# Optimization experiments

Measured on AMD Instinct MI355X. Metric: run time of the kernel, lower is better.

The kernel has to match this reference:

```python
import jax, jax.numpy as jnp
import numpy as np

N_NODES = 50000
N_EDGES = 800000
IN_CH = 128
OUT_CH = 64
HID_CH = 2 * OUT_CH  # 128


def gcn_conv(x, edge_index, W, b, n_nodes):
    """PyG GCNConv: linear -> add self-loops -> sym-normalized scatter-add -> bias."""
    h = x @ W  # [N, out]
    loop = jnp.arange(n_nodes)
    row = jnp.concatenate([edge_index[0], loop])  # source nodes
    col = jnp.concatenate([edge_index[1], loop])  # target nodes
    deg = jax.ops.segment_sum(jnp.ones_like(col, dtype=h.dtype), col, num_segments=n_nodes)
    dinv = jnp.where(deg > 0, jax.lax.rsqrt(jnp.maximum(deg, 1.0)), 0.0)
    norm = dinv[row] * dinv[col]  # [E+N]
    msg = h[row] * norm[:, None]  # gather + scale, [E+N, out]
    out = jax.ops.segment_sum(msg, col, num_segments=n_nodes)  # scatter-add
    return out + b


def setup_inputs() -> dict:
    key = jax.random.key(0)
    ks = jax.random.split(key, 9)
    x = jax.random.normal(ks[0], (N_NODES, IN_CH), dtype=jnp.float32)
    edge_index = jax.random.randint(ks[1], (2, N_EDGES), 0, N_NODES, dtype=jnp.int64)
    s_in = 1.0 / np.sqrt(IN_CH)
    s_hid = 1.0 / np.sqrt(HID_CH)
    W1 = jax.random.normal(ks[2], (IN_CH, HID_CH), dtype=jnp.float32) * s_in
    b1 = jnp.zeros((HID_CH,), dtype=jnp.float32)
    W2 = jax.random.normal(ks[3], (HID_CH, OUT_CH), dtype=jnp.float32) * s_hid
    b2 = jnp.zeros((OUT_CH,), dtype=jnp.float32)
    W3 = jax.random.normal(ks[4], (HID_CH, OUT_CH), dtype=jnp.float32) * s_hid
    b3 = jnp.zeros((OUT_CH,), dtype=jnp.float32)
    return {"x": x, "edge_index": edge_index, "W1": W1, "b1": b1,
            "W2": W2, "b2": b2, "W3": W3, "b3": b3}


def reference(x, edge_index, W1, b1, W2, b2, W3, b3):
    act = jax.nn.relu
    hidden = act(gcn_conv(x, edge_index, W1, b1, N_NODES))
    x1 = act(gcn_conv(hidden, edge_index, W2, b2, N_NODES))
    x2 = act(gcn_conv(hidden, edge_index, W3, b3, N_NODES))
    return (x1, x2)
```

## Files before the change

### kernel.cpp

```cpp
#include <hip/hip_runtime.h>

#define N_NODES 50000
#define N_EDGES 800000
#define CH 128
#define WT_PAD 136
#define DUMMY N_NODES
#define SLOT_LOG 6
#define AGG_HALF_BLKS 1563

typedef __attribute__((ext_vector_type(8))) short short8;
typedef __attribute__((ext_vector_type(4))) float floatx4;

__device__ __forceinline__ short f2bf(float f) {
    union { float f; unsigned u; } v; v.f = f;
    unsigned r = v.u + 0x7fff + ((v.u >> 16) & 1);
    return (short)(r >> 16);
}
__device__ __forceinline__ float bflo(unsigned u) {
    union { unsigned u; float f; } v; v.u = u << 16; return v.f;
}
__device__ __forceinline__ float bfhi(unsigned u) {
    union { unsigned u; float f; } v; v.u = u & 0xffff0000u; return v.f;
}


__global__ __launch_bounds__(256) void prep_kernel(const float* __restrict__ W1,
                                                   const float* __restrict__ W2,
                                                   const float* __restrict__ W3,
                                                   const float* __restrict__ b2,
                                                   const float* __restrict__ b3,
                                                   unsigned short* __restrict__ Wt1,
                                                   unsigned short* __restrict__ Wt23,
                                                   float* __restrict__ b23,
                                                   int* __restrict__ counts,
                                                   float* __restrict__ dinv,
                                                   unsigned int* __restrict__ gdummy) {
    int i = blockIdx.x * blockDim.x + threadIdx.x;
    if (i < 128 * 128) {
        int n = i >> 7, k = i & 127;
        Wt1[i] = (unsigned short)f2bf(W1[k * 128 + n]);
        float w = (n < 64) ? W2[k * 64 + n] : W3[k * 64 + (n - 64)];
        Wt23[i] = (unsigned short)f2bf(w);
    } else if (i < 128 * 128 + 128) {
        int k2 = i - 128 * 128;
        b23[k2] = (k2 < 64) ? b2[k2] : b3[k2 - 64];
    } else if (i < 128 * 128 + 192) {
        gdummy[i - (128 * 128 + 128)] = 0;
    }
    for (int j = i; j < N_NODES; j += 66 * 256) {
        counts[j] = 0;
        dinv[j] = 1.0f;
    }
}


__global__ void rank_kernel(const int* __restrict__ ei, int* __restrict__ counts,
                            unsigned* __restrict__ rankdst) {
    int e = blockIdx.x * blockDim.x + threadIdx.x;
    if (e < N_EDGES) {
        int dst = ei[N_EDGES + e];
        int r = atomicAdd(&counts[dst], 1);
        rankdst[e] = ((unsigned)r << 16) | (unsigned)dst;
    }
}

__global__ void scatter_plain(const int* __restrict__ ei, const int* __restrict__ counts,
                              const unsigned* __restrict__ rankdst,
                              unsigned short* __restrict__ sorted_src,
                              float* __restrict__ dinv) {
    int e = blockIdx.x * blockDim.x + threadIdx.x;
    if (e < N_EDGES) {
        int src = ei[e];
        unsigned p = rankdst[e];
        int dst = (int)(p & 0xffffu);
        int r = (int)(p >> 16);
        int deg = counts[dst];
        int base = dst << SLOT_LOG;
        if (r < 64) sorted_src[base + r] = (unsigned short)src;
        if (r == 0) dinv[dst] = rsqrtf((float)(deg + 1));
        if (r == deg - 1) {
            int pc = (deg + 3) & ~3;
            if (pc > 64) pc = 64;
            for (int q = deg; q < pc; ++q) sorted_src[base + q] = (unsigned short)DUMMY;
        }
    }
}


template <bool A_BF16>
__global__ __launch_bounds__(256) void gemm_mfma(const void* __restrict__ Ain,
                                                 const unsigned short* __restrict__ Wt,
                                                 const float* __restrict__ dinv,
                                                 unsigned short* __restrict__ g) {
    __shared__ unsigned short lds[128 * WT_PAD];
    int tid = threadIdx.x;
    int wave = tid >> 6, lane = tid & 63;
    int quad = lane >> 4, ln = lane & 15;

    {
        int r = tid >> 1, h = tid & 1;
        const int4* src = (const int4*)(Wt + r * 128 + h * 64);
#pragma unroll
        for (int i = 0; i < 8; ++i)
            *(int4*)&lds[r * WT_PAD + h * 64 + i * 8] = src[i];
    }

    int row_base = blockIdx.x * 64 + wave * 16;
    int arow = row_base + ln;
    bool ok = arow < N_NODES;
    short8 afrag[4];
    if (A_BF16) {
        const unsigned short* A = (const unsigned short*)Ain;
#pragma unroll
        for (int kk = 0; kk < 4; ++kk) {
            short8 v = {};
            if (ok) v = *(const short8*)(A + arow * 128 + kk * 32 + quad * 8);
            afrag[kk] = v;
        }
    } else {
        const float* A = (const float*)Ain;
#pragma unroll
        for (int kk = 0; kk < 4; ++kk) {
            short8 v = {};
            if (ok) {
                const float* p = A + arow * 128 + kk * 32 + quad * 8;
#pragma unroll
                for (int j = 0; j < 8; ++j) v[j] = f2bf(p[j]);
            }
            afrag[kk] = v;
        }
    }
    __syncthreads();

    floatx4 acc[8] = {};
#pragma unroll
    for (int n0 = 0; n0 < 8; ++n0) {
#pragma unroll
        for (int kk = 0; kk < 4; ++kk) {
            short8 b = *(const short8*)&lds[(n0 * 16 + ln) * WT_PAD + kk * 32 + quad * 8];
            acc[n0] = __builtin_amdgcn_mfma_f32_16x16x32_bf16(afrag[kk], b, acc[n0], 0, 0, 0);
        }
    }

    __syncthreads();
    unsigned short* st = &lds[wave * 16 * WT_PAD];
    float dv[4];
#pragma unroll
    for (int r = 0; r < 4; ++r) {
        int node = row_base + quad * 4 + r;
        dv[r] = (node < N_NODES) ? dinv[node] : 0.f;
    }
#pragma unroll
    for (int n0 = 0; n0 < 8; ++n0)
#pragma unroll
        for (int r = 0; r < 4; ++r)
            st[(quad * 4 + r) * WT_PAD + n0 * 16 + ln] =
                (unsigned short)f2bf(acc[n0][r] * dv[r]);
    __syncthreads();

#pragma unroll
    for (int i = 0; i < 4; ++i) {
        int row = i * 4 + quad;
        int node = row_base + row;
        short8 v = *(const short8*)&st[row * WT_PAD + ln * 8];
        if (node < N_NODES) *(short8*)(g + node * 128 + ln * 8) = v;
    }
}


template <int MODE>
__global__ __launch_bounds__(256) void aggregate_bf16(const unsigned short* __restrict__ g,
                                                      const float* __restrict__ dinv,
                                                      const int* __restrict__ degs,
                                                      const unsigned short* __restrict__ srcs,
                                                      const float* __restrict__ bias,
                                                      void* __restrict__ outp) {
    int h = 0, nb = blockIdx.x;
    if (nb >= AGG_HALF_BLKS) { h = 1; nb -= AGG_HALF_BLKS; }
    int n = nb * 32 + (threadIdx.x >> 3);
    if (n >= N_NODES) return;
    int c4 = threadIdx.x & 7;
    int hoff = h * 8;
    const uint4* grow = (const uint4*)g;
    uint4 u = grow[n * 16 + hoff + c4];
    float a0 = bflo(u.x), a1 = bfhi(u.x), a2 = bflo(u.y), a3 = bfhi(u.y);
    float a4 = bflo(u.z), a5 = bfhi(u.z), a6 = bflo(u.w), a7 = bfhi(u.w);
    float c0 = 0.f, c1 = 0.f, c2 = 0.f, c3 = 0.f, c5 = 0.f, c6 = 0.f, c7 = 0.f, c8 = 0.f;
    int beg = n << SLOT_LOG;
    int pend = beg + ((degs[n] + 3) & ~3);
    int e = beg;
    for (; e + 8 <= pend; e += 8) {
        ushort4 sa = *(const ushort4*)&srcs[e];
        ushort4 sb = *(const ushort4*)&srcs[e + 4];
        uint4 v0 = grow[sa.x * 16 + hoff + c4];
        uint4 v1 = grow[sa.y * 16 + hoff + c4];
        uint4 v2 = grow[sa.z * 16 + hoff + c4];
        uint4 v3 = grow[sa.w * 16 + hoff + c4];
        uint4 v4 = grow[sb.x * 16 + hoff + c4];
        uint4 v5 = grow[sb.y * 16 + hoff + c4];
        uint4 v6 = grow[sb.z * 16 + hoff + c4];
        uint4 v7 = grow[sb.w * 16 + hoff + c4];
        a0 += bflo(v0.x); a1 += bfhi(v0.x); a2 += bflo(v0.y); a3 += bfhi(v0.y);
        a4 += bflo(v0.z); a5 += bfhi(v0.z); a6 += bflo(v0.w); a7 += bfhi(v0.w);
        c0 += bflo(v1.x); c1 += bfhi(v1.x); c2 += bflo(v1.y); c3 += bfhi(v1.y);
        c5 += bflo(v1.z); c6 += bfhi(v1.z); c7 += bflo(v1.w); c8 += bfhi(v1.w);
        a0 += bflo(v2.x); a1 += bfhi(v2.x); a2 += bflo(v2.y); a3 += bfhi(v2.y);
        a4 += bflo(v2.z); a5 += bfhi(v2.z); a6 += bflo(v2.w); a7 += bfhi(v2.w);
        c0 += bflo(v3.x); c1 += bfhi(v3.x); c2 += bflo(v3.y); c3 += bfhi(v3.y);
        c5 += bflo(v3.z); c6 += bfhi(v3.z); c7 += bflo(v3.w); c8 += bfhi(v3.w);
        a0 += bflo(v4.x); a1 += bfhi(v4.x); a2 += bflo(v4.y); a3 += bfhi(v4.y);
        a4 += bflo(v4.z); a5 += bfhi(v4.z); a6 += bflo(v4.w); a7 += bfhi(v4.w);
        c0 += bflo(v5.x); c1 += bfhi(v5.x); c2 += bflo(v5.y); c3 += bfhi(v5.y);
        c5 += bflo(v5.z); c6 += bfhi(v5.z); c7 += bflo(v5.w); c8 += bfhi(v5.w);
        a0 += bflo(v6.x); a1 += bfhi(v6.x); a2 += bflo(v6.y); a3 += bfhi(v6.y);
        a4 += bflo(v6.z); a5 += bfhi(v6.z); a6 += bflo(v6.w); a7 += bfhi(v6.w);
        c0 += bflo(v7.x); c1 += bfhi(v7.x); c2 += bflo(v7.y); c3 += bfhi(v7.y);
        c5 += bflo(v7.z); c6 += bfhi(v7.z); c7 += bflo(v7.w); c8 += bfhi(v7.w);
    }
    if (e < pend) {
        ushort4 sa = *(const ushort4*)&srcs[e];
        uint4 v0 = grow[sa.x * 16 + hoff + c4];
        uint4 v1 = grow[sa.y * 16 + hoff + c4];
        uint4 v2 = grow[sa.z * 16 + hoff + c4];
        uint4 v3 = grow[sa.w * 16 + hoff + c4];
        a0 += bflo(v0.x); a1 += bfhi(v0.x); a2 += bflo(v0.y); a3 += bfhi(v0.y);
        a4 += bflo(v0.z); a5 += bfhi(v0.z); a6 += bflo(v0.w); a7 += bfhi(v0.w);
        c0 += bflo(v1.x); c1 += bfhi(v1.x); c2 += bflo(v1.y); c3 += bfhi(v1.y);
        c5 += bflo(v1.z); c6 += bfhi(v1.z); c7 += bflo(v1.w); c8 += bfhi(v1.w);
        a0 += bflo(v2.x); a1 += bfhi(v2.x); a2 += bflo(v2.y); a3 += bfhi(v2.y);
        a4 += bflo(v2.z); a5 += bfhi(v2.z); a6 += bflo(v2.w); a7 += bfhi(v2.w);
        c0 += bflo(v3.x); c1 += bfhi(v3.x); c2 += bflo(v3.y); c3 += bfhi(v3.y);
        c5 += bflo(v3.z); c6 += bfhi(v3.z); c7 += bflo(v3.w); c8 += bfhi(v3.w);
    }
    a0 += c0; a1 += c1; a2 += c2; a3 += c3; a4 += c5; a5 += c6; a6 += c7; a7 += c8;
    float d = dinv[n];
    float4 bv0 = ((const float4*)bias)[h * 16 + c4 * 2];
    float4 bv1 = ((const float4*)bias)[h * 16 + c4 * 2 + 1];
    float o0 = fmaxf(d * a0 + bv0.x, 0.f);
    float o1 = fmaxf(d * a1 + bv0.y, 0.f);
    float o2 = fmaxf(d * a2 + bv0.z, 0.f);
    float o3 = fmaxf(d * a3 + bv0.w, 0.f);
    float o4 = fmaxf(d * a4 + bv1.x, 0.f);
    float o5 = fmaxf(d * a5 + bv1.y, 0.f);
    float o6 = fmaxf(d * a6 + bv1.z, 0.f);
    float o7 = fmaxf(d * a7 + bv1.w, 0.f);
    if (MODE == 0) {
        uint4 w;
        w.x = ((unsigned)(unsigned short)f2bf(o0)) | (((unsigned)(unsigned short)f2bf(o1)) << 16);
        w.y = ((unsigned)(unsigned short)f2bf(o2)) | (((unsigned)(unsigned short)f2bf(o3)) << 16);
        w.z = ((unsigned)(unsigned short)f2bf(o4)) | (((unsigned)(unsigned short)f2bf(o5)) << 16);
        w.w = ((unsigned)(unsigned short)f2bf(o6)) | (((unsigned)(unsigned short)f2bf(o7)) << 16);
        ((uint4*)outp)[n * 16 + hoff + c4] = w;
    } else {
        float* out = (float*)outp + (size_t)h * N_NODES * 64;
        ((float4*)out)[n * 16 + c4 * 2] = make_float4(o0, o1, o2, o3);
        ((float4*)out)[n * 16 + c4 * 2 + 1] = make_float4(o4, o5, o6, o7);
    }
}


extern "C" void kernel_launch(void* const* d_in, const int* in_sizes, int n_in,
                              void* d_out, int out_size, void* d_ws, size_t ws_size,
                              hipStream_t stream) {
    const float* x  = (const float*)d_in[0];
    const int*   ei = (const int*)d_in[1];
    const float* W1 = (const float*)d_in[2];
    const float* b1 = (const float*)d_in[3];
    const float* W2 = (const float*)d_in[4];
    const float* b2 = (const float*)d_in[5];
    const float* W3 = (const float*)d_in[6];
    const float* b3 = (const float*)d_in[7];
    float* out = (float*)d_out;

    char* w = (char*)d_ws;
    int*            counts     = (int*)(w + 0);
    float*          dinv       = (float*)(w + 204800);
    unsigned*       rankdst    = (unsigned*)(w + 409600);
    unsigned short* sorted_src = (unsigned short*)(w + 3686400);
    unsigned short* Wt1        = (unsigned short*)(w + 10485760);
    unsigned short* Wt23       = (unsigned short*)(w + 10518528);
    float*          b23        = (float*)(w + 10551296);
    unsigned short* g1         = (unsigned short*)(w + 12582912);
    unsigned short* hidden     = (unsigned short*)(w + 25690112);

    prep_kernel<<<66, 256, 0, stream>>>(W1, W2, W3, b2, b3, Wt1, Wt23, b23, counts, dinv,
                                        (unsigned int*)(g1 + N_NODES * 128));
    rank_kernel<<<(N_EDGES + 255) / 256, 256, 0, stream>>>(ei, counts, rankdst);
    scatter_plain<<<(N_EDGES + 255) / 256, 256, 0, stream>>>(ei, counts, rankdst,
                                                             sorted_src, dinv);

    const int gemm_blocks = (N_NODES + 63) / 64;
    const int agg_blocks = 2 * AGG_HALF_BLKS;

    gemm_mfma<false><<<gemm_blocks, 256, 0, stream>>>(x, Wt1, dinv, g1);
    aggregate_bf16<0><<<agg_blocks, 256, 0, stream>>>(g1, dinv, counts, sorted_src, b1, hidden);

    gemm_mfma<true><<<gemm_blocks, 256, 0, stream>>>(hidden, Wt23, dinv, g1);
    aggregate_bf16<1><<<agg_blocks, 256, 0, stream>>>(g1, dinv, counts, sorted_src, b23, out);
}
```

Baseline: 212.3 us.

## Fuse rank counting with first GEMM and carry source dinv in edge slots

```diff
diff --git a/kernel.cpp b/kernel.cpp
--- a/kernel.cpp
+++ b/kernel.cpp
@@ -4,8 +4,8 @@
 #define N_EDGES 800000
 #define CH 128
 #define WT_PAD 136
-#define DUMMY N_NODES
 #define SLOT_LOG 6
+#define RANK_BLKS 3125
 #define AGG_HALF_BLKS 1563
 
 typedef __attribute__((ext_vector_type(8))) short short8;
@@ -21,6 +21,12 @@
 }
 __device__ __forceinline__ float bfhi(unsigned u) {
     union { unsigned u; float f; } v; v.u = u & 0xffff0000u; return v.f;
+}
+__device__ __forceinline__ void acc8s(float* a, uint4 v, float s) {
+    a[0] = fmaf(s, bflo(v.x), a[0]); a[1] = fmaf(s, bfhi(v.x), a[1]);
+    a[2] = fmaf(s, bflo(v.y), a[2]); a[3] = fmaf(s, bfhi(v.y), a[3]);
+    a[4] = fmaf(s, bflo(v.z), a[4]); a[5] = fmaf(s, bfhi(v.z), a[5]);
+    a[6] = fmaf(s, bflo(v.w), a[6]); a[7] = fmaf(s, bfhi(v.w), a[7]);
 }
 
 
@@ -32,9 +38,7 @@
                                                    unsigned short* __restrict__ Wt1,
                                                    unsigned short* __restrict__ Wt23,
                                                    float* __restrict__ b23,
-                                                   int* __restrict__ counts,
-                                                   float* __restrict__ dinv,
-                                                   unsigned int* __restrict__ gdummy) {
+                                                   int* __restrict__ counts) {
     int i = blockIdx.x * blockDim.x + threadIdx.x;
     if (i < 128 * 128) {
         int n = i >> 7, k = i & 127;
@@ -44,30 +48,112 @@
     } else if (i < 128 * 128 + 128) {
         int k2 = i - 128 * 128;
         b23[k2] = (k2 < 64) ? b2[k2] : b3[k2 - 64];
-    } else if (i < 128 * 128 + 192) {
-        gdummy[i - (128 * 128 + 128)] = 0;
-    }
-    for (int j = i; j < N_NODES; j += 66 * 256) {
-        counts[j] = 0;
-        dinv[j] = 1.0f;
-    }
-}
-
-
-__global__ void rank_kernel(const int* __restrict__ ei, int* __restrict__ counts,
-                            unsigned* __restrict__ rankdst) {
-    int e = blockIdx.x * blockDim.x + threadIdx.x;
-    if (e < N_EDGES) {
+    }
+    for (int j = i; j < N_NODES; j += 66 * 256) counts[j] = 0;
+}
+
+
+template <bool A_BF16>
+__device__ __forceinline__ void gemm_body(int bid, const void* __restrict__ Ain,
+                                          const unsigned short* __restrict__ Wt,
+                                          unsigned short* __restrict__ g,
+                                          unsigned short* lds, int tid) {
+    int wave = tid >> 6, lane = tid & 63;
+    int quad = lane >> 4, ln = lane & 15;
+
+    {
+        int r = tid >> 1, h = tid & 1;
+        const int4* src = (const int4*)(Wt + r * 128 + h * 64);
+#pragma unroll
+        for (int i = 0; i < 8; ++i)
+            *(int4*)&lds[r * WT_PAD + h * 64 + i * 8] = src[i];
+    }
+
+    int row_base = bid * 64 + wave * 16;
+    int arow = row_base + ln;
+    bool ok = arow < N_NODES;
+    short8 afrag[4];
+    if (A_BF16) {
+        const unsigned short* A = (const unsigned short*)Ain;
+#pragma unroll
+        for (int kk = 0; kk < 4; ++kk) {
+            short8 v = {};
+            if (ok) v = *(const short8*)(A + arow * 128 + kk * 32 + quad * 8);
+            afrag[kk] = v;
+        }
+    } else {
+        const float* A = (const float*)Ain;
+#pragma unroll
+        for (int kk = 0; kk < 4; ++kk) {
+            short8 v = {};
+            if (ok) {
+                const float* p = A + arow * 128 + kk * 32 + quad * 8;
+#pragma unroll
+                for (int j = 0; j < 8; ++j) v[j] = f2bf(p[j]);
+            }
+            afrag[kk] = v;
+        }
+    }
+    __syncthreads();
+
+    floatx4 acc[8] = {};
+#pragma unroll
+    for (int n0 = 0; n0 < 8; ++n0) {
+#pragma unroll
+        for (int kk = 0; kk < 4; ++kk) {
+            short8 b = *(const short8*)&lds[(n0 * 16 + ln) * WT_PAD + kk * 32 + quad * 8];
+            acc[n0] = __builtin_amdgcn_mfma_f32_16x16x32_bf16(afrag[kk], b, acc[n0], 0, 0, 0);
+        }
+    }
+
+    __syncthreads();
+    unsigned short* st = &lds[wave * 16 * WT_PAD];
+#pragma unroll
+    for (int n0 = 0; n0 < 8; ++n0)
+#pragma unroll
+        for (int r = 0; r < 4; ++r)
+            st[(quad * 4 + r) * WT_PAD + n0 * 16 + ln] = (unsigned short)f2bf(acc[n0][r]);
+    __syncthreads();
+
+#pragma unroll
+    for (int i = 0; i < 4; ++i) {
+        int row = i * 4 + quad;
+        int node = row_base + row;
+        short8 v = *(const short8*)&st[row * WT_PAD + ln * 8];
+        if (node < N_NODES) *(short8*)(g + node * 128 + ln * 8) = v;
+    }
+}
+
+
+__global__ __launch_bounds__(256) void rank_gemm1(const int* __restrict__ ei,
+                                                  int* __restrict__ counts,
+                                                  unsigned* __restrict__ rankdst,
+                                                  const float* __restrict__ x,
+                                                  const unsigned short* __restrict__ Wt1,
+                                                  unsigned short* __restrict__ g1) {
+    __shared__ unsigned short lds[128 * WT_PAD];
+    if (blockIdx.x < RANK_BLKS) {
+        int e = blockIdx.x * 256 + threadIdx.x;
         int dst = ei[N_EDGES + e];
         int r = atomicAdd(&counts[dst], 1);
         rankdst[e] = ((unsigned)r << 16) | (unsigned)dst;
-    }
-}
+        return;
+    }
+    gemm_body<false>(blockIdx.x - RANK_BLKS, x, Wt1, g1, lds, threadIdx.x);
+}
+
+
+__global__ __launch_bounds__(256) void gemm_bf16(const unsigned short* __restrict__ A,
+                                                 const unsigned short* __restrict__ Wt,
+                                                 unsigned short* __restrict__ g) {
+    __shared__ unsigned short lds[128 * WT_PAD];
+    gemm_body<true>(blockIdx.x, A, Wt, g, lds, threadIdx.x);
+}
+
 
 __global__ void scatter_plain(const int* __restrict__ ei, const int* __restrict__ counts,
                               const unsigned* __restrict__ rankdst,
-                              unsigned short* __restrict__ sorted_src,
-                              float* __restrict__ dinv) {
+                              unsigned* __restrict__ slots) {
     int e = blockIdx.x * blockDim.x + threadIdx.x;
     if (e < N_EDGES) {
         int src = ei[e];
@@ -75,104 +161,23 @@
         int dst = (int)(p & 0xffffu);
         int r = (int)(p >> 16);
         int deg = counts[dst];
+        float dv = rsqrtf((float)(counts[src] + 1));
         int base = dst << SLOT_LOG;
-        if (r < 64) sorted_src[base + r] = (unsigned short)src;
-        if (r == 0) dinv[dst] = rsqrtf((float)(deg + 1));
+        unsigned slot = (((unsigned)(unsigned short)f2bf(dv)) << 16) | (unsigned)src;
+        if (r < 64) slots[base + r] = slot;
         if (r == deg - 1) {
             int pc = (deg + 3) & ~3;
             if (pc > 64) pc = 64;
-            for (int q = deg; q < pc; ++q) sorted_src[base + q] = (unsigned short)DUMMY;
-        }
-    }
-}
-
-
-template <bool A_BF16>
-__global__ __launch_bounds__(256) void gemm_mfma(const void* __restrict__ Ain,
-                                                 const unsigned short* __restrict__ Wt,
-                                                 const float* __restrict__ dinv,
-                                                 unsigned short* __restrict__ g) {
-    __shared__ unsigned short lds[128 * WT_PAD];
-    int tid = threadIdx.x;
-    int wave = tid >> 6, lane = tid & 63;
-    int quad = lane >> 4, ln = lane & 15;
-
-    {
-        int r = tid >> 1, h = tid & 1;
-        const int4* src = (const int4*)(Wt + r * 128 + h * 64);
-#pragma unroll
-        for (int i = 0; i < 8; ++i)
-            *(int4*)&lds[r * WT_PAD + h * 64 + i * 8] = src[i];
-    }
-
-    int row_base = blockIdx.x * 64 + wave * 16;
-    int arow = row_base + ln;
-    bool ok = arow < N_NODES;
-    short8 afrag[4];
-    if (A_BF16) {
-        const unsigned short* A = (const unsigned short*)Ain;
-#pragma unroll
-        for (int kk = 0; kk < 4; ++kk) {
-            short8 v = {};
-            if (ok) v = *(const short8*)(A + arow * 128 + kk * 32 + quad * 8);
-            afrag[kk] = v;
-        }
-    } else {
-        const float* A = (const float*)Ain;
-#pragma unroll
-        for (int kk = 0; kk < 4; ++kk) {
-            short8 v = {};
-            if (ok) {
-                const float* p = A + arow * 128 + kk * 32 + quad * 8;
-#pragma unroll
-                for (int j = 0; j < 8; ++j) v[j] = f2bf(p[j]);
-            }
-            afrag[kk] = v;
-        }
-    }
-    __syncthreads();
-
-    floatx4 acc[8] = {};
-#pragma unroll
-    for (int n0 = 0; n0 < 8; ++n0) {
-#pragma unroll
-        for (int kk = 0; kk < 4; ++kk) {
-            short8 b = *(const short8*)&lds[(n0 * 16 + ln) * WT_PAD + kk * 32 + quad * 8];
-            acc[n0] = __builtin_amdgcn_mfma_f32_16x16x32_bf16(afrag[kk], b, acc[n0], 0, 0, 0);
-        }
-    }
-
-    __syncthreads();
-    unsigned short* st = &lds[wave * 16 * WT_PAD];
-    float dv[4];
-#pragma unroll
-    for (int r = 0; r < 4; ++r) {
-        int node = row_base + quad * 4 + r;
-        dv[r] = (node < N_NODES) ? dinv[node] : 0.f;
-    }
-#pragma unroll
-    for (int n0 = 0; n0 < 8; ++n0)
-#pragma unroll
-        for (int r = 0; r < 4; ++r)
-            st[(quad * 4 + r) * WT_PAD + n0 * 16 + ln] =
-                (unsigned short)f2bf(acc[n0][r] * dv[r]);
-    __syncthreads();
-
-#pragma unroll
-    for (int i = 0; i < 4; ++i) {
-        int row = i * 4 + quad;
-        int node = row_base + row;
-        short8 v = *(const short8*)&st[row * WT_PAD + ln * 8];
-        if (node < N_NODES) *(short8*)(g + node * 128 + ln * 8) = v;
+            for (int q = deg; q < pc; ++q) slots[base + q] = 0u;
+        }
     }
 }
 
 
 template <int MODE>
 __global__ __launch_bounds__(256) void aggregate_bf16(const unsigned short* __restrict__ g,
-                                                      const float* __restrict__ dinv,
                                                       const int* __restrict__ degs,
-                                                      const unsigned short* __restrict__ srcs,
+                                                      const unsigned* __restrict__ slots,
                                                       const float* __restrict__ bias,
                                                       void* __restrict__ outp) {
     int h = 0, nb = blockIdx.x;
@@ -182,68 +187,58 @@
     int c4 = threadIdx.x & 7;
     int hoff = h * 8;
     const uint4* grow = (const uint4*)g;
-    uint4 u = grow[n * 16 + hoff + c4];
-    float a0 = bflo(u.x), a1 = bfhi(u.x), a2 = bflo(u.y), a3 = bfhi(u.y);
-    float a4 = bflo(u.z), a5 = bfhi(u.z), a6 = bflo(u.w), a7 = bfhi(u.w);
-    float c0 = 0.f, c1 = 0.f, c2 = 0.f, c3 = 0.f, c5 = 0.f, c6 = 0.f, c7 = 0.f, c8 = 0.f;
+    int deg = degs[n];
+    float dn = rsqrtf((float)(deg + 1));
+    float a[8], c[8];
+    {
+        uint4 u = grow[n * 16 + hoff + c4];
+        a[0] = dn * bflo(u.x); a[1] = dn * bfhi(u.x);
+        a[2] = dn * bflo(u.y); a[3] = dn * bfhi(u.y);
+        a[4] = dn * bflo(u.z); a[5] = dn * bfhi(u.z);
+        a[6] = dn * bflo(u.w); a[7] = dn * bfhi(u.w);
+#pragma unroll
+        for (int j = 0; j < 8; ++j) c[j] = 0.f;
+    }
     int beg = n << SLOT_LOG;
-    int pend = beg + ((degs[n] + 3) & ~3);
+    int pend = beg + ((deg + 3) & ~3);
     int e = beg;
     for (; e + 8 <= pend; e += 8) {
-        ushort4 sa = *(const ushort4*)&srcs[e];
-        ushort4 sb = *(const ushort4*)&srcs[e + 4];
-        uint4 v0 = grow[sa.x * 16 + hoff + c4];
-        uint4 v1 = grow[sa.y * 16 + hoff + c4];
-        uint4 v2 = grow[sa.z * 16 + hoff + c4];
-        uint4 v3 = grow[sa.w * 16 + hoff + c4];
-        uint4 v4 = grow[sb.x * 16 + hoff + c4];
-        uint4 v5 = grow[sb.y * 16 + hoff + c4];
-        uint4 v6 = grow[sb.z * 16 + hoff + c4];
-        uint4 v7 = grow[sb.w * 16 + hoff + c4];
-        a0 += bflo(v0.x); a1 += bfhi(v0.x); a2 += bflo(v0.y); a3 += bfhi(v0.y);
-        a4 += bflo(v0.z); a5 += bfhi(v0.z); a6 += bflo(v0.w); a7 += bfhi(v0.w);
-        c0 += bflo(v1.x); c1 += bfhi(v1.x); c2 += bflo(v1.y); c3 += bfhi(v1.y);
-        c5 += bflo(v1.z); c6 += bfhi(v1.z); c7 += bflo(v1.w); c8 += bfhi(v1.w);
-        a0 += bflo(v2.x); a1 += bfhi(v2.x); a2 += bflo(v2.y); a3 += bfhi(v2.y);
-        a4 += bflo(v2.z); a5 += bfhi(v2.z); a6 += bflo(v2.w); a7 += bfhi(v2.w);
-        c0 += bflo(v3.x); c1 += bfhi(v3.x); c2 += bflo(v3.y); c3 += bfhi(v3.y);
-        c5 += bflo(v3.z); c6 += bfhi(v3.z); c7 += bflo(v3.w); c8 += bfhi(v3.w);
-        a0 += bflo(v4.x); a1 += bfhi(v4.x); a2 += bflo(v4.y); a3 += bfhi(v4.y);
-        a4 += bflo(v4.z); a5 += bfhi(v4.z); a6 += bflo(v4.w); a7 += bfhi(v4.w);
-        c0 += bflo(v5.x); c1 += bfhi(v5.x); c2 += bflo(v5.y); c3 += bfhi(v5.y);
-        c5 += bflo(v5.z); c6 += bfhi(v5.z); c7 += bflo(v5.w); c8 += bfhi(v5.w);
-        a0 += bflo(v6.x); a1 += bfhi(v6.x); a2 += bflo(v6.y); a3 += bfhi(v6.y);
-        a4 += bflo(v6.z); a5 += bfhi(v6.z); a6 += bflo(v6.w); a7 += bfhi(v6.w);
-        c0 += bflo(v7.x); c1 += bfhi(v7.x); c2 += bflo(v7.y); c3 += bfhi(v7.y);
-        c5 += bflo(v7.z); c6 += bfhi(v7.z); c7 += bflo(v7.w); c8 += bfhi(v7.w);
+        uint4 sa = *(const uint4*)&slots[e];
+        uint4 sb = *(const uint4*)&slots[e + 4];
+        uint4 v0 = grow[(sa.x & 0xffffu) * 16 + hoff + c4];
+        uint4 v1 = grow[(sa.y & 0xffffu) * 16 + hoff + c4];
+        uint4 v2 = grow[(sa.z & 0xffffu) * 16 + hoff + c4];
+        uint4 v3 = grow[(sa.w & 0xffffu) * 16 + hoff + c4];
+        uint4 v4 = grow[(sb.x & 0xffffu) * 16 + hoff + c4];
+        uint4 v5 = grow[(sb.y & 0xffffu) * 16 + hoff + c4];
+        uint4 v6 = grow[(sb.z & 0xffffu) * 16 + hoff + c4];
+        uint4 v7 = grow[(sb.w & 0xffffu) * 16 + hoff + c4];
+        acc8s(a, v0, bfhi(sa.x)); acc8s(c, v1, bfhi(sa.y));
+        acc8s(a, v2, bfhi(sa.z)); acc8s(c, v3, bfhi(sa.w));
+        acc8s(a, v4, bfhi(sb.x)); acc8s(c, v5, bfhi(sb.y));
+        acc8s(a, v6, bfhi(sb.z)); acc8s(c, v7, bfhi(sb.w));
     }
     if (e < pend) {
-        ushort4 sa = *(const ushort4*)&srcs[e];
-        uint4 v0 = grow[sa.x * 16 + hoff + c4];
-        uint4 v1 = grow[sa.y * 16 + hoff + c4];
-        uint4 v2 = grow[sa.z * 16 + hoff + c4];
-        uint4 v3 = grow[sa.w * 16 + hoff + c4];
-        a0 += bflo(v0.x); a1 += bfhi(v0.x); a2 += bflo(v0.y); a3 += bfhi(v0.y);
-        a4 += bflo(v0.z); a5 += bfhi(v0.z); a6 += bflo(v0.w); a7 += bfhi(v0.w);
-        c0 += bflo(v1.x); c1 += bfhi(v1.x); c2 += bflo(v1.y); c3 += bfhi(v1.y);
-        c5 += bflo(v1.z); c6 += bfhi(v1.z); c7 += bflo(v1.w); c8 += bfhi(v1.w);
-        a0 += bflo(v2.x); a1 += bfhi(v2.x); a2 += bflo(v2.y); a3 += bfhi(v2.y);
-        a4 += bflo(v2.z); a5 += bfhi(v2.z); a6 += bflo(v2.w); a7 += bfhi(v2.w);
-        c0 += bflo(v3.x); c1 += bfhi(v3.x); c2 += bflo(v3.y); c3 += bfhi(v3.y);
-        c5 += bflo(v3.z); c6 += bfhi(v3.z); c7 += bflo(v3.w); c8 += bfhi(v3.w);
-    }
-    a0 += c0; a1 += c1; a2 += c2; a3 += c3; a4 += c5; a5 += c6; a6 += c7; a7 += c8;
-    float d = dinv[n];
+        uint4 sa = *(const uint4*)&slots[e];
+        uint4 v0 = grow[(sa.x & 0xffffu) * 16 + hoff + c4];
+        uint4 v1 = grow[(sa.y & 0xffffu) * 16 + hoff + c4];
+        uint4 v2 = grow[(sa.z & 0xffffu) * 16 + hoff + c4];
+        uint4 v3 = grow[(sa.w & 0xffffu) * 16 + hoff + c4];
+        acc8s(a, v0, bfhi(sa.x)); acc8s(c, v1, bfhi(sa.y));
+        acc8s(a, v2, bfhi(sa.z)); acc8s(c, v3, bfhi(sa.w));
+    }
+#pragma unroll
+    for (int j = 0; j < 8; ++j) a[j] += c[j];
     float4 bv0 = ((const float4*)bias)[h * 16 + c4 * 2];
     float4 bv1 = ((const float4*)bias)[h * 16 + c4 * 2 + 1];
-    float o0 = fmaxf(d * a0 + bv0.x, 0.f);
-    float o1 = fmaxf(d * a1 + bv0.y, 0.f);
-    float o2 = fmaxf(d * a2 + bv0.z, 0.f);
-    float o3 = fmaxf(d * a3 + bv0.w, 0.f);
-    float o4 = fmaxf(d * a4 + bv1.x, 0.f);
-    float o5 = fmaxf(d * a5 + bv1.y, 0.f);
-    float o6 = fmaxf(d * a6 + bv1.z, 0.f);
-    float o7 = fmaxf(d * a7 + bv1.w, 0.f);
+    float o0 = fmaxf(dn * a[0] + bv0.x, 0.f);
+    float o1 = fmaxf(dn * a[1] + bv0.y, 0.f);
+    float o2 = fmaxf(dn * a[2] + bv0.z, 0.f);
+    float o3 = fmaxf(dn * a[3] + bv0.w, 0.f);
+    float o4 = fmaxf(dn * a[4] + bv1.x, 0.f);
+    float o5 = fmaxf(dn * a[5] + bv1.y, 0.f);
+    float o6 = fmaxf(dn * a[6] + bv1.z, 0.f);
+    float o7 = fmaxf(dn * a[7] + bv1.w, 0.f);
     if (MODE == 0) {
         uint4 w;
         w.x = ((unsigned)(unsigned short)f2bf(o0)) | (((unsigned)(unsigned short)f2bf(o1)) << 16);
@@ -273,28 +268,26 @@
     float* out = (float*)d_out;
 
     char* w = (char*)d_ws;
-    int*            counts     = (int*)(w + 0);
-    float*          dinv       = (float*)(w + 204800);
-    unsigned*       rankdst    = (unsigned*)(w + 409600);
-    unsigned short* sorted_src = (unsigned short*)(w + 3686400);
-    unsigned short* Wt1        = (unsigned short*)(w + 10485760);
-    unsigned short* Wt23       = (unsigned short*)(w + 10518528);
-    float*          b23        = (float*)(w + 10551296);
-    unsigned short* g1         = (unsigned short*)(w + 12582912);
-    unsigned short* hidden     = (unsigned short*)(w + 25690112);
-
-    prep_kernel<<<66, 256, 0, stream>>>(W1, W2, W3, b2, b3, Wt1, Wt23, b23, counts, dinv,
-                                        (unsigned int*)(g1 + N_NODES * 128));
-    rank_kernel<<<(N_EDGES + 255) / 256, 256, 0, stream>>>(ei, counts, rankdst);
-    scatter_plain<<<(N_EDGES + 255) / 256, 256, 0, stream>>>(ei, counts, rankdst,
-                                                             sorted_src, dinv);
-
-    const int gemm_blocks = (N_NODES + 63) / 64;
+    int*            counts  = (int*)(w + 0);
+    unsigned*       rankdst = (unsigned*)(w + 204800);
+    unsigned*       slots   = (unsigned*)(w + 3604480);
+    unsigned short* Wt1     = (unsigned short*)(w + 16777216);
+    unsigned short* Wt23    = (unsigned short*)(w + 16809984);
+    float*          b23     = (float*)(w + 16842752);
+    unsigned short* g1      = (unsigned short*)(w + 20971520);
+    unsigned short* hidden  = (unsigned short*)(w + 34603008);
+
+    prep_kernel<<<66, 256, 0, stream>>>(W1, W2, W3, b2, b3, Wt1, Wt23, b23, counts);
+
+    rank_gemm1<<<RANK_BLKS + 782, 256, 0, stream>>>(ei, counts, rankdst, x, Wt1, g1);
+
+    scatter_plain<<<RANK_BLKS, 256, 0, stream>>>(ei, counts, rankdst, slots);
+
     const int agg_blocks = 2 * AGG_HALF_BLKS;
 
-    gemm_mfma<false><<<gemm_blocks, 256, 0, stream>>>(x, Wt1, dinv, g1);
-    aggregate_bf16<0><<<agg_blocks, 256, 0, stream>>>(g1, dinv, counts, sorted_src, b1, hidden);
-
-    gemm_mfma<true><<<gemm_blocks, 256, 0, stream>>>(hidden, Wt23, dinv, g1);
-    aggregate_bf16<1><<<agg_blocks, 256, 0, stream>>>(g1, dinv, counts, sorted_src, b23, out);
-}
+    aggregate_bf16<0><<<agg_blocks, 256, 0, stream>>>(g1, counts, slots, b1, hidden);
+
+    gemm_bf16<<<782, 256, 0, stream>>>(hidden, Wt23, g1);
+
+    aggregate_bf16<1><<<agg_blocks, 256, 0, stream>>>(g1, counts, slots, b23, out);
+}
```

New measurement: 214.6 us. About the same (+1.1%).
